# Performance work log

Measured on AMD Instinct MI355X. Metric: run time of the kernel, lower is better.

Reference implementation:

```python
import jax, jax.numpy as jnp
import numpy as np

B, DX, DZ, DY = 8192, 512, 1024, 256


def setup_inputs() -> dict:
    key = jax.random.key(0)
    ks = jax.random.split(key, 13)
    s = 0.02
    return {
        "xs": jax.random.normal(ks[0], (B, DX), dtype=jnp.float32),
        "Wx": jax.random.normal(ks[1], (DZ, DX), dtype=jnp.float32) * s,
        "bx": jnp.zeros((DZ,), dtype=jnp.float32),
        "Wy": jax.random.normal(ks[2], (DZ, DY), dtype=jnp.float32) * s,
        "by": jnp.zeros((DZ,), dtype=jnp.float32),
        "Wn": jax.random.normal(ks[3], (DZ, 3 * DZ), dtype=jnp.float32) * s,
        "bn": jnp.zeros((DZ,), dtype=jnp.float32),
        "Wu": jax.random.normal(ks[4], (DY, DZ), dtype=jnp.float32) * s,
        "bu": jnp.zeros((DY,), dtype=jnp.float32),
        "Wq": jax.random.normal(ks[5], (DY, DZ), dtype=jnp.float32) * s,
        "bq": jnp.zeros((DY,), dtype=jnp.float32),
        "ys_init": jax.random.normal(ks[6], (B, DY), dtype=jnp.float32),
        "zs_init": jax.random.normal(ks[7], (B, DZ), dtype=jnp.float32),
        "T": 4,
        "n": 6,
    }


def reference(xs, Wx, bx, Wy, by, Wn, bn, Wu, bu, Wq, bq, ys_init, zs_init, T, n):
    xs_e = xs @ Wx.T + bx                      # [B, DZ]
    ys_e = ys_init @ Wy.T + by                 # [B, DZ]
    zs = zs_init                               # [B, DZ]
    null = jnp.zeros_like(xs_e)

    def query(x, y, z):
        w = jnp.concatenate([x, y, z], axis=-1)  # [B, 3*DZ]
        return jnp.tanh(w @ Wn.T + bn)

    # no-grad refinement (T-1 outer iterations)
    for _ in range(T - 1):
        for _ in range(n):
            zs = query(xs_e, ys_e, zs)
        ys_e = query(null, ys_e, zs)
    ys_e = jax.lax.stop_gradient(ys_e)
    zs = jax.lax.stop_gradient(zs)

    # final grad-enabled block
    for _ in range(n):
        zs = query(xs_e, ys_e, zs)
    ys_e = query(null, ys_e, zs)

    y_hat = jax.nn.sigmoid(ys_e @ Wu.T + bu)
    q_hat = jax.nn.sigmoid(ys_e @ Wq.T + bq)
    return (y_hat, q_hat)
```

## Files before the change

### kernel.cpp

```cpp
#include <hip/hip_runtime.h>
#include <hip/hip_bf16.h>
#include <cstdint>
#include <cstddef>

#define B_   8192
#define DX_  512
#define DZ_  1024
#define DY_  256
#define T_   4
#define NN_  6

typedef float f32x4 __attribute__((ext_vector_type(4)));
typedef short s16x8 __attribute__((ext_vector_type(8)));
typedef __hip_bfloat16 bf16;

__device__ __forceinline__ void gload_lds16(const bf16* g, void* l) {
  __builtin_amdgcn_global_load_lds(
      (const __attribute__((address_space(1))) void*)g,
      (__attribute__((address_space(3))) void*)l,
      16, 0, 0);
}

__device__ __forceinline__ float bf2f(unsigned short u) {
  union { unsigned int i; float f; } cv; cv.i = ((unsigned int)u) << 16; return cv.f;
}

__device__ __forceinline__ void cv4(const float* __restrict__ s, bf16* __restrict__ d, long i) {
  float4 v = ((const float4*)s)[i];
  ushort4 o;
  bf16 a0 = __float2bfloat16(v.x); o.x = *(unsigned short*)&a0;
  bf16 a1 = __float2bfloat16(v.y); o.y = *(unsigned short*)&a1;
  bf16 a2 = __float2bfloat16(v.z); o.z = *(unsigned short*)&a2;
  bf16 a3 = __float2bfloat16(v.w); o.w = *(unsigned short*)&a3;
  ((ushort4*)d)[i] = o;
}

__global__ void cvt_all_kernel(const float* __restrict__ Wn, const float* __restrict__ Wx,
                               const float* __restrict__ Wy, const float* __restrict__ Wu,
                               const float* __restrict__ Wq, const float* __restrict__ xs,
                               const float* __restrict__ ys0, const float* __restrict__ zs0,
                               const float* __restrict__ bu, const float* __restrict__ bq,
                               bf16* __restrict__ Wn_b, bf16* __restrict__ Wx_b,
                               bf16* __restrict__ Wy_b, bf16* __restrict__ Wuq_b,
                               bf16* __restrict__ xs_b, bf16* __restrict__ ysin_b,
                               bf16* __restrict__ z_a, float* __restrict__ buq) {
  const long NWN = (long)DZ_ * 3 * DZ_ / 4, NWX = (long)DZ_ * DX_ / 4,
             NWY = (long)DZ_ * DY_ / 4,     NWU = (long)DY_ * DZ_ / 4,
             NXS = (long)B_ * DX_ / 4,      NYS = (long)B_ * DY_ / 4,
             NZS = (long)B_ * DZ_ / 4,      NBQ = 2 * DY_ / 4;
  const long total = NWN + NWX + NWY + 2 * NWU + NXS + NYS + NZS + NBQ;
  for (long i = (long)blockIdx.x * blockDim.x + threadIdx.x; i < total;
       i += (long)gridDim.x * blockDim.x) {
    long j = i;
    if (j < NWN) { cv4(Wn, Wn_b, j); continue; } j -= NWN;
    if (j < NWX) { cv4(Wx, Wx_b, j); continue; } j -= NWX;
    if (j < NWY) { cv4(Wy, Wy_b, j); continue; } j -= NWY;
    if (j < NWU) { cv4(Wu, Wuq_b, j); continue; } j -= NWU;
    if (j < NWU) { cv4(Wq, Wuq_b + (size_t)DY_ * DZ_ / 4 * 4, j); continue; } j -= NWU;
    if (j < NXS) { cv4(xs, xs_b, j); continue; } j -= NXS;
    if (j < NYS) { cv4(ys0, ysin_b, j); continue; } j -= NYS;
    if (j < NZS) { cv4(zs0, z_a, j); continue; } j -= NZS;
    float4 v;
    if (j < DY_ / 4) v = ((const float4*)bu)[j];
    else             v = ((const float4*)bq)[j - DY_ / 4];
    ((float4*)buq)[j] = v;
  }
}

template<int ACT, int MODE, bool HASADD>
__global__ __launch_bounds__(512, 2)
void gemm_bt(const bf16* __restrict__ A, int lda,
             const bf16* __restrict__ W, int ldw,
             const float* __restrict__ bias,
             const bf16* __restrict__ add1,
             bf16* __restrict__ out_pre,
             void* __restrict__ out, void* __restrict__ out2,
             int N, int K)
{
  __shared__ __align__(16) char ldsc[3 * 49152];
  const int t    = threadIdx.x;
  const int lane = t & 63;
  const int wave = t >> 6;
  const int m0 = blockIdx.x * 256;
  const int n0 = blockIdx.y * 128;

  const int srow = t >> 3;
  const int q    = (t & 7) ^ ((t >> 3) & 7);
  const bf16* gA = A + (size_t)(m0 + srow) * lda + q * 8;
  const bf16* gB = W + (size_t)(n0 + srow) * ldw + q * 8;
  const int wb = wave * 1024;

  auto stage = [&](int kt) {
    char* base = ldsc + (kt % 3) * 49152;
    const int ko = kt << 6;
#pragma unroll
    for (int i = 0; i < 4; ++i)
      gload_lds16(gA + (size_t)(i * 64) * lda + ko, base + i * 8192 + wb);
#pragma unroll
    for (int i = 0; i < 2; ++i)
      gload_lds16(gB + (size_t)(i * 64) * ldw + ko, base + 32768 + i * 8192 + wb);
  };

  const int mo = (wave >> 1) * 64;
  const int no = (wave & 1) * 64;
  const int fr = lane & 15;
  const int g4 = lane >> 4;
  const int rb = g4 * 4;

  const int NT = K >> 6;

  float bv[4] = {0.f, 0.f, 0.f, 0.f};
  if (bias) {
#pragma unroll
    for (int j = 0; j < 4; ++j) bv[j] = bias[n0 + no + j * 16 + fr];
  }
  unsigned short adr[4][4][4];
  if (HASADD && MODE != 1) {
#pragma unroll
    for (int f = 0; f < 4; ++f)
#pragma unroll
      for (int j = 0; j < 4; ++j) {
        const unsigned short* p = (const unsigned short*)add1
            + (size_t)(m0 + mo + f * 16 + rb) * N + (n0 + no + j * 16 + fr);
#pragma unroll
        for (int r = 0; r < 4; ++r) adr[f][j][r] = p[(size_t)r * N];
      }
  }
  __builtin_amdgcn_sched_barrier(0);
  stage(0);
  stage(1);
  __builtin_amdgcn_sched_barrier(0);

  f32x4 acc[4][4];
#pragma unroll
  for (int f = 0; f < 4; ++f)
#pragma unroll
    for (int j = 0; j < 4; ++j)
#pragma unroll
      for (int r = 0; r < 4; ++r) {
        float v = bv[j];
        if (HASADD && MODE != 1) v += bf2f(adr[f][j][r]);
        acc[f][j][r] = v;
      }

  s16x8 a0[4], b0[4], a1[4], b1[4];
  auto ldfrags = [&](int kt, int s, s16x8* fa, s16x8* fb) {
    const char* pA = ldsc + (kt % 3) * 49152;
    const char* pB = pA + 32768;
    const int cb = ((s * 4 + g4) ^ (fr & 7)) * 16;
#pragma unroll
    for (int f = 0; f < 4; ++f) fa[f] = *(const s16x8*)(pA + (mo + f * 16 + fr) * 128 + cb);
#pragma unroll
    for (int j = 0; j < 4; ++j) fb[j] = *(const s16x8*)(pB + (no + j * 16 + fr) * 128 + cb);
  };
  auto domfma = [&](const s16x8* fa, const s16x8* fb) {
    __builtin_amdgcn_s_setprio(1);
#pragma unroll
    for (int f = 0; f < 4; ++f)
#pragma unroll
      for (int j = 0; j < 4; ++j)
        acc[f][j] = __builtin_amdgcn_mfma_f32_16x16x32_bf16(fa[f], fb[j], acc[f][j], 0, 0, 0);
    __builtin_amdgcn_s_setprio(0);
  };

  asm volatile("s_waitcnt vmcnt(6)" ::: "memory");
  __builtin_amdgcn_s_barrier();
  __builtin_amdgcn_sched_barrier(0);

  for (int kt = 0; kt < NT; ++kt) {
    ldfrags(kt, 0, a0, b0);
    ldfrags(kt, 1, a1, b1);
    if (kt + 2 < NT) stage(kt + 2);
    __builtin_amdgcn_sched_barrier(0);
    asm volatile("s_waitcnt lgkmcnt(8)" ::: "memory");
    __builtin_amdgcn_sched_barrier(0);
    domfma(a0, b0);
    asm volatile("s_waitcnt lgkmcnt(0)" ::: "memory");
    __builtin_amdgcn_sched_barrier(0);
    domfma(a1, b1);
    if (kt + 2 < NT)      asm volatile("s_waitcnt vmcnt(6)" ::: "memory");
    else if (kt + 1 < NT) asm volatile("s_waitcnt vmcnt(0)" ::: "memory");
    if (kt + 1 < NT) {
      __builtin_amdgcn_s_barrier();
      __builtin_amdgcn_sched_barrier(0);
    }
  }

#pragma unroll
  for (int f = 0; f < 4; ++f) {
#pragma unroll
    for (int j = 0; j < 4; ++j) {
      const int n = n0 + no + j * 16 + fr;
#pragma unroll
      for (int r = 0; r < 4; ++r) {
        const int m = m0 + mo + f * 16 + rb + r;
        float v = acc[f][j][r];
        if (MODE == 1) {
          out_pre[(size_t)m * N + n] = __float2bfloat16(v);
          v += bf2f(((const unsigned short*)add1)[(size_t)m * N + n]);
        }
        if (ACT == 1)      { float e = __expf(2.f * v); v = 1.f - 2.f / (e + 1.f); }
        else if (ACT == 2) v = 1.f / (1.f + __expf(-v));
        if (MODE == 2) {
          if (n < DY_) ((float*)out)[(size_t)m * DY_ + n] = v;
          else         ((float*)out2)[(size_t)m * DY_ + (n - DY_)] = v;
        } else {
          ((bf16*)out)[(size_t)m * N + n] = __float2bfloat16(v);
        }
      }
    }
  }
}

extern "C" void kernel_launch(void* const* d_in, const int* in_sizes, int n_in,
                              void* d_out, int out_size, void* d_ws, size_t ws_size,
                              hipStream_t stream) {
  const float* xs  = (const float*)d_in[0];
  const float* Wx  = (const float*)d_in[1];
  const float* bx  = (const float*)d_in[2];
  const float* Wy  = (const float*)d_in[3];
  const float* by  = (const float*)d_in[4];
  const float* Wn  = (const float*)d_in[5];
  const float* bn  = (const float*)d_in[6];
  const float* Wu  = (const float*)d_in[7];
  const float* bu  = (const float*)d_in[8];
  const float* Wq  = (const float*)d_in[9];
  const float* bq  = (const float*)d_in[10];
  const float* ys0 = (const float*)d_in[11];
  const float* zs0 = (const float*)d_in[12];

  char* ws = (char*)d_ws;
  size_t off = 0;
  auto take = [&](size_t bytes) -> char* {
    char* p = ws + off;
    off += (bytes + 255) & ~(size_t)255;
    return p;
  };

  bf16*  Wn_b   = (bf16*)take((size_t)DZ_ * 3 * DZ_ * 2);
  bf16*  Wx_b   = (bf16*)take((size_t)DZ_ * DX_ * 2);
  bf16*  Wy_b   = (bf16*)take((size_t)DZ_ * DY_ * 2);
  bf16*  Wuq_b  = (bf16*)take((size_t)2 * DY_ * DZ_ * 2);
  float* buq    = (float*)take((size_t)2 * DY_ * 4);
  bf16*  ys_b   = (bf16*)take((size_t)B_ * DZ_ * 2);
  bf16*  z_a    = (bf16*)take((size_t)B_ * DZ_ * 2);
  bf16*  z_b    = (bf16*)take((size_t)B_ * DZ_ * 2);
  bf16*  cx     = (bf16*)take((size_t)B_ * DZ_ * 2);
  bf16*  cy     = (bf16*)take((size_t)B_ * DZ_ * 2);
  bf16*  c      = (bf16*)take((size_t)B_ * DZ_ * 2);
  bf16* xs_b   = c;
  bf16* ysin_b = (bf16*)((char*)c + (size_t)B_ * DX_ * 2);
  bf16* xse_b  = cy;

  cvt_all_kernel<<<2048, 256, 0, stream>>>(Wn, Wx, Wy, Wu, Wq, xs, ys0, zs0, bu, bq,
                                           Wn_b, Wx_b, Wy_b, Wuq_b,
                                           xs_b, ysin_b, z_a, buq);

  const dim3 blk(512);
  const dim3 gz(B_ / 256, DZ_ / 128);
  const dim3 gh(B_ / 256, 4);

  gemm_bt<0, 0, false><<<gz, blk, 0, stream>>>(xs_b, DX_, Wx_b, DX_, bx, nullptr, nullptr, xse_b, nullptr, DZ_, DX_);
  gemm_bt<0, 0, false><<<gz, blk, 0, stream>>>(ysin_b, DY_, Wy_b, DY_, by, nullptr, nullptr, ys_b, nullptr, DZ_, DY_);
  gemm_bt<0, 0, false><<<gz, blk, 0, stream>>>(xse_b, DZ_, Wn_b, 3 * DZ_, nullptr, nullptr, nullptr, cx, nullptr, DZ_, DZ_);

  bf16* zc = z_a;
  bf16* zn = z_b;
  for (int tt = 0; tt < T_; ++tt) {
    gemm_bt<0, 1, true><<<gz, blk, 0, stream>>>(ys_b, DZ_, Wn_b + DZ_, 3 * DZ_, bn, cx, cy, c, nullptr, DZ_, DZ_);
    for (int i = 0; i < NN_; ++i) {
      gemm_bt<1, 0, true><<<gz, blk, 0, stream>>>(zc, DZ_, Wn_b + 2 * DZ_, 3 * DZ_, nullptr, c, nullptr, zn, nullptr, DZ_, DZ_);
      bf16* tmp = zc; zc = zn; zn = tmp;
    }
    gemm_bt<1, 0, true><<<gz, blk, 0, stream>>>(zc, DZ_, Wn_b + 2 * DZ_, 3 * DZ_, nullptr, cy, nullptr, ys_b, nullptr, DZ_, DZ_);
  }

  float* outp = (float*)d_out;
  gemm_bt<2, 2, false><<<gh, blk, 0, stream>>>(ys_b, DZ_, Wuq_b, DZ_, buq, nullptr, nullptr,
                                               outp, outp + (size_t)B_ * DY_, 2 * DY_, DZ_);
}
```

Baseline: 924.6 us.

## Run early-iteration z recurrence GEMMs in FP8 with swizzled layout

Adds a dedicated FP8 MFMA GEMM with fused tanh for the z-update recurrence in the first T-1 outer iterations. The z-weight slice of Wn and the initial z are converted to FP8 in a swizzled column order that suits the LDS reads. Each step writes FP8 output, plus a bf16 copy on the last inner step so the existing bf16 kernels can continue. The final grad block keeps bf16. The goal is to raise matrix throughput and halve operand traffic on most of the dominant GEMMs, at the cost of FP8 rounding on the recurrent state and weights, which risks accuracy.

```diff
diff --git a/kernel.cpp b/kernel.cpp
--- a/kernel.cpp
+++ b/kernel.cpp
@@ -12,9 +12,10 @@
 
 typedef float f32x4 __attribute__((ext_vector_type(4)));
 typedef short s16x8 __attribute__((ext_vector_type(8)));
+typedef long i64x2 __attribute__((ext_vector_type(2)));
 typedef __hip_bfloat16 bf16;
 
-__device__ __forceinline__ void gload_lds16(const bf16* g, void* l) {
+__device__ __forceinline__ void gload_lds16(const void* g, void* l) {
   __builtin_amdgcn_global_load_lds(
       (const __attribute__((address_space(1))) void*)g,
       (__attribute__((address_space(3))) void*)l,
@@ -23,6 +24,10 @@
 
 __device__ __forceinline__ float bf2f(unsigned short u) {
   union { unsigned int i; float f; } cv; cv.i = ((unsigned int)u) << 16; return cv.f;
+}
+
+__device__ __forceinline__ int permb(int n) {
+  return (n & ~63) | (((n >> 3) & 3) << 4) | (((n >> 5) & 1) << 3) | (n & 7);
 }
 
 __device__ __forceinline__ void cv4(const float* __restrict__ s, bf16* __restrict__ d, long i) {
@@ -34,6 +39,13 @@
   bf16 a3 = __float2bfloat16(v.w); o.w = *(unsigned short*)&a3;
   ((ushort4*)d)[i] = o;
 }
+__device__ __forceinline__ void cv4f8(const float* __restrict__ src, unsigned char* __restrict__ dst,
+                                      long row, int k0, int srcld, int srcoff) {
+  float4 v = *(const float4*)(src + row * srcld + srcoff + k0);
+  int p = __builtin_amdgcn_cvt_pk_fp8_f32(v.x, v.y, 0, 0);
+  p = __builtin_amdgcn_cvt_pk_fp8_f32(v.z, v.w, p, 1);
+  *(int*)(dst + row * DZ_ + permb(k0)) = p;
+}
 
 __global__ void cvt_all_kernel(const float* __restrict__ Wn, const float* __restrict__ Wx,
                                const float* __restrict__ Wy, const float* __restrict__ Wu,
@@ -43,12 +55,14 @@
                                bf16* __restrict__ Wn_b, bf16* __restrict__ Wx_b,
                                bf16* __restrict__ Wy_b, bf16* __restrict__ Wuq_b,
                                bf16* __restrict__ xs_b, bf16* __restrict__ ysin_b,
-                               bf16* __restrict__ z_a, float* __restrict__ buq) {
+                               bf16* __restrict__ z_a, float* __restrict__ buq,
+                               unsigned char* __restrict__ Wnz8, unsigned char* __restrict__ z_a8) {
   const long NWN = (long)DZ_ * 3 * DZ_ / 4, NWX = (long)DZ_ * DX_ / 4,
              NWY = (long)DZ_ * DY_ / 4,     NWU = (long)DY_ * DZ_ / 4,
              NXS = (long)B_ * DX_ / 4,      NYS = (long)B_ * DY_ / 4,
-             NZS = (long)B_ * DZ_ / 4,      NBQ = 2 * DY_ / 4;
-  const long total = NWN + NWX + NWY + 2 * NWU + NXS + NYS + NZS + NBQ;
+             NZS = (long)B_ * DZ_ / 4,      NBQ = 2 * DY_ / 4,
+             NW8 = (long)DZ_ * DZ_ / 4,     NZ8 = (long)B_ * DZ_ / 4;
+  const long total = NWN + NWX + NWY + 2 * NWU + NXS + NYS + NZS + NBQ + NW8 + NZ8;
   for (long i = (long)blockIdx.x * blockDim.x + threadIdx.x; i < total;
        i += (long)gridDim.x * blockDim.x) {
     long j = i;
@@ -56,14 +70,22 @@
     if (j < NWX) { cv4(Wx, Wx_b, j); continue; } j -= NWX;
     if (j < NWY) { cv4(Wy, Wy_b, j); continue; } j -= NWY;
     if (j < NWU) { cv4(Wu, Wuq_b, j); continue; } j -= NWU;
-    if (j < NWU) { cv4(Wq, Wuq_b + (size_t)DY_ * DZ_ / 4 * 4, j); continue; } j -= NWU;
+    if (j < NWU) { cv4(Wq, Wuq_b + (size_t)DY_ * DZ_, j); continue; } j -= NWU;
     if (j < NXS) { cv4(xs, xs_b, j); continue; } j -= NXS;
     if (j < NYS) { cv4(ys0, ysin_b, j); continue; } j -= NYS;
     if (j < NZS) { cv4(zs0, z_a, j); continue; } j -= NZS;
-    float4 v;
-    if (j < DY_ / 4) v = ((const float4*)bu)[j];
-    else             v = ((const float4*)bq)[j - DY_ / 4];
-    ((float4*)buq)[j] = v;
+    if (j < NBQ) {
+      float4 v = (j < DY_ / 4) ? ((const float4*)bu)[j] : ((const float4*)bq)[j - DY_ / 4];
+      ((float4*)buq)[j] = v; continue;
+    } j -= NBQ;
+    if (j < NW8) {
+      long e = j * 4; long row = e >> 10; int k0 = (int)(e & 1023);
+      cv4f8(Wn, Wnz8, row, k0, 3 * DZ_, 2 * DZ_); continue;
+    } j -= NW8;
+    {
+      long e = j * 4; long row = e >> 10; int k0 = (int)(e & 1023);
+      cv4f8(zs0, z_a8, row, k0, DZ_, 0);
+    }
   }
 }
 
@@ -212,6 +234,119 @@
   }
 }
 
+__global__ __launch_bounds__(512, 2)
+void gemm_f8(const unsigned char* __restrict__ A8,
+             const unsigned char* __restrict__ W8,
+             const bf16* __restrict__ add1,
+             unsigned char* __restrict__ out8,
+             bf16* __restrict__ out16)
+{
+  __shared__ __align__(16) char ldsc[4 * 24576];
+  const int t    = threadIdx.x;
+  const int lane = t & 63;
+  const int wave = t >> 6;
+  const int m0 = blockIdx.x * 256;
+  const int n0 = blockIdx.y * 128;
+
+  const int srow = t >> 2;
+  const int q    = (t & 3) ^ ((t >> 3) & 3);
+  const unsigned char* gA = A8 + (size_t)(m0 + srow) * DZ_ + q * 16;
+  const unsigned char* gB = W8 + (size_t)(n0 + srow) * DZ_ + q * 16;
+  const int wb = wave * 1024;
+
+  auto stage = [&](int kt) {
+    char* base = ldsc + (kt & 3) * 24576;
+    const int ko = kt << 6;
+    gload_lds16(gA + ko, base + wb);
+    gload_lds16(gA + (size_t)128 * DZ_ + ko, base + 8192 + wb);
+    gload_lds16(gB + ko, base + 16384 + wb);
+  };
+
+  const int mo = (wave >> 1) * 64;
+  const int no = (wave & 1) * 64;
+  const int fr = lane & 15;
+  const int g4 = lane >> 4;
+  const int rb = g4 * 4;
+  const int cb = (g4 ^ ((fr >> 1) & 3)) * 16;
+
+  const int NT = DZ_ >> 6;
+
+  unsigned short adr[4][4][4];
+#pragma unroll
+  for (int f = 0; f < 4; ++f)
+#pragma unroll
+    for (int j = 0; j < 4; ++j) {
+      const unsigned short* p = (const unsigned short*)add1
+          + (size_t)(m0 + mo + f * 16 + rb) * DZ_ + (n0 + no + j * 16 + fr);
+#pragma unroll
+      for (int r = 0; r < 4; ++r) adr[f][j][r] = p[(size_t)r * DZ_];
+    }
+  __builtin_amdgcn_sched_barrier(0);
+  stage(0); stage(1); stage(2);
+  __builtin_amdgcn_sched_barrier(0);
+
+  f32x4 acc[4][4];
+#pragma unroll
+  for (int f = 0; f < 4; ++f)
+#pragma unroll
+    for (int j = 0; j < 4; ++j)
+#pragma unroll
+      for (int r = 0; r < 4; ++r) acc[f][j][r] = bf2f(adr[f][j][r]);
+
+  asm volatile("s_waitcnt vmcnt(6)" ::: "memory");
+  __builtin_amdgcn_s_barrier();
+  __builtin_amdgcn_sched_barrier(0);
+
+  for (int kt = 0; kt < NT; ++kt) {
+    const char* pA = ldsc + (kt & 3) * 24576;
+    const char* pB = pA + 16384;
+    i64x2 av[4], bv[4];
+#pragma unroll
+    for (int f = 0; f < 4; ++f) av[f] = *(const i64x2*)(pA + (mo + f * 16 + fr) * 64 + cb);
+#pragma unroll
+    for (int j = 0; j < 4; ++j) bv[j] = *(const i64x2*)(pB + (no + j * 16 + fr) * 64 + cb);
+    if (kt + 3 < NT) stage(kt + 3);
+    __builtin_amdgcn_sched_barrier(0);
+    asm volatile("s_waitcnt lgkmcnt(0)" ::: "memory");
+    __builtin_amdgcn_sched_barrier(0);
+    __builtin_amdgcn_s_setprio(1);
+#pragma unroll
+    for (int f = 0; f < 4; ++f)
+#pragma unroll
+      for (int j = 0; j < 4; ++j) {
+        acc[f][j] = __builtin_amdgcn_mfma_f32_16x16x32_fp8_fp8(av[f][0], bv[j][0], acc[f][j], 0, 0, 0);
+        acc[f][j] = __builtin_amdgcn_mfma_f32_16x16x32_fp8_fp8(av[f][1], bv[j][1], acc[f][j], 0, 0, 0);
+      }
+    __builtin_amdgcn_s_setprio(0);
+    const int rem = NT - 1 - kt;
+    if (rem >= 3)      asm volatile("s_waitcnt vmcnt(6)" ::: "memory");
+    else if (rem == 2) asm volatile("s_waitcnt vmcnt(3)" ::: "memory");
+    else if (rem == 1) asm volatile("s_waitcnt vmcnt(0)" ::: "memory");
+    if (rem >= 1) {
+      __builtin_amdgcn_s_barrier();
+      __builtin_amdgcn_sched_barrier(0);
+    }
+  }
+
+#pragma unroll
+  for (int f = 0; f < 4; ++f) {
+#pragma unroll
+    for (int j = 0; j < 4; ++j) {
+      const int n = n0 + no + j * 16 + fr;
+      const int np = permb(n);
+#pragma unroll
+      for (int r = 0; r < 4; ++r) {
+        const int m = m0 + mo + f * 16 + rb + r;
+        float v = acc[f][j][r];
+        float e = __expf(2.f * v); v = 1.f - 2.f / (e + 1.f);
+        out8[(size_t)m * DZ_ + np] =
+            (unsigned char)__builtin_amdgcn_cvt_pk_fp8_f32(v, v, 0, 0);
+        if (out16) out16[(size_t)m * DZ_ + n] = __float2bfloat16(v);
+      }
+    }
+  }
+}
+
 extern "C" void kernel_launch(void* const* d_in, const int* in_sizes, int n_in,
                               void* d_out, int out_size, void* d_ws, size_t ws_size,
                               hipStream_t stream) {
@@ -248,13 +383,16 @@
   bf16*  cx     = (bf16*)take((size_t)B_ * DZ_ * 2);
   bf16*  cy     = (bf16*)take((size_t)B_ * DZ_ * 2);
   bf16*  c      = (bf16*)take((size_t)B_ * DZ_ * 2);
+  unsigned char* Wnz8 = (unsigned char*)take((size_t)DZ_ * DZ_);
+  unsigned char* z_a8 = (unsigned char*)take((size_t)B_ * DZ_);
+  unsigned char* z_b8 = (unsigned char*)take((size_t)B_ * DZ_);
   bf16* xs_b   = c;
   bf16* ysin_b = (bf16*)((char*)c + (size_t)B_ * DX_ * 2);
   bf16* xse_b  = cy;
 
   cvt_all_kernel<<<2048, 256, 0, stream>>>(Wn, Wx, Wy, Wu, Wq, xs, ys0, zs0, bu, bq,
                                            Wn_b, Wx_b, Wy_b, Wuq_b,
-                                           xs_b, ysin_b, z_a, buq);
+                                           xs_b, ysin_b, z_a, buq, Wnz8, z_a8);
 
   const dim3 blk(512);
   const dim3 gz(B_ / 256, DZ_ / 128);
@@ -266,11 +404,21 @@
 
   bf16* zc = z_a;
   bf16* zn = z_b;
+  unsigned char* zc8 = z_a8;
+  unsigned char* zn8 = z_b8;
   for (int tt = 0; tt < T_; ++tt) {
     gemm_bt<0, 1, true><<<gz, blk, 0, stream>>>(ys_b, DZ_, Wn_b + DZ_, 3 * DZ_, bn, cx, cy, c, nullptr, DZ_, DZ_);
-    for (int i = 0; i < NN_; ++i) {
-      gemm_bt<1, 0, true><<<gz, blk, 0, stream>>>(zc, DZ_, Wn_b + 2 * DZ_, 3 * DZ_, nullptr, c, nullptr, zn, nullptr, DZ_, DZ_);
+    if (tt < T_ - 1) {
+      for (int i = 0; i < NN_; ++i) {
+        gemm_f8<<<gz, blk, 0, stream>>>(zc8, Wnz8, c, zn8, (i == NN_ - 1) ? zn : nullptr);
+        unsigned char* t8 = zc8; zc8 = zn8; zn8 = t8;
+      }
       bf16* tmp = zc; zc = zn; zn = tmp;
+    } else {
+      for (int i = 0; i < NN_; ++i) {
+        gemm_bt<1, 0, true><<<gz, blk, 0, stream>>>(zc, DZ_, Wn_b + 2 * DZ_, 3 * DZ_, nullptr, c, nullptr, zn, nullptr, DZ_, DZ_);
+        bf16* tmp = zc; zc = zn; zn = tmp;
+      }
     }
     gemm_bt<1, 0, true><<<gz, blk, 0, stream>>>(zc, DZ_, Wn_b + 2 * DZ_, 3 * DZ_, nullptr, cy, nullptr, ys_b, nullptr, DZ_, DZ_);
   }
```

New measurement: 828.9 us. -10.4%, faster.
